# Kernel tuning notes

Hardware: AMD Instinct MI355X
Metric: run time of the kernel (lower is better)

## Reference

```python
import math
import jax, jax.numpy as jnp
import numpy as np

LMAX = 10
R_REF = 6371000.0
N = 1_000_000


def _sh_renorm(l, m, fourpi=True):
    base = math.sqrt((2.0 * l + 1.0) * math.factorial(l - abs(m)) / (4.0 * math.pi * math.factorial(l + abs(m))))
    if fourpi:
        base *= math.sqrt(4.0 * math.pi)
    return base


def _assoc_legendre(l, m, x):
    # P_l^m(x) via the standard stable recursion; l, m are Python ints (unrolled at trace time).
    pmm = jnp.ones_like(x)
    if m > 0:
        somx2 = jnp.sqrt(jnp.clip((1.0 - x) * (1.0 + x), 0.0, None))
        fact = 1.0
        for _ in range(1, m + 1):
            pmm = pmm * (-fact) * somx2
            fact += 2.0
    if l == m:
        return pmm
    pmmp1 = x * (2.0 * m + 1.0) * pmm
    if l == m + 1:
        return pmmp1
    pll = pmmp1
    for ll in range(m + 2, l + 1):
        pll = ((2.0 * ll - 1.0) * x * pmmp1 - (ll + m - 1.0) * pmm) / (ll - m)
        pmm = pmmp1
        pmmp1 = pll
    return pll


def _sh(m, l, phi, theta):
    cos_theta = jnp.clip(jnp.cos(theta), -1.0 + 1e-07, 1.0 - 1e-07)
    P_lm = _assoc_legendre(l, abs(m), cos_theta)
    K_lm = _sh_renorm(l, m)
    if m == 0:
        return K_lm * P_lm
    elif m > 0:
        return math.sqrt(2.0) * K_lm * jnp.cos(m * phi) * P_lm
    else:
        return math.sqrt(2.0) * K_lm * jnp.sin(-m * phi) * P_lm


def setup_inputs() -> dict:
    key = jax.random.key(0)
    k1, k2, k3 = jax.random.split(key, 3)
    lon = jax.random.uniform(k1, (N,), jnp.float32, -180.0, 180.0)
    lat = jax.random.uniform(k2, (N,), jnp.float32, -89.0, 89.0)
    r = R_REF * (1.0 + 0.01 * jax.random.uniform(k3, (N,), jnp.float32))
    return {"lonlatr": jnp.stack([lon, lat, r], axis=-1)}


def reference(lonlatr):
    lon, lat, r = lonlatr[:, 0], lonlatr[:, 1], lonlatr[:, 2]
    phi = jnp.deg2rad(lon + 180.0)
    theta = jnp.clip(jnp.deg2rad(90.0 - lat), 1e-07, math.pi - 1e-07)
    Y = []
    for l in range(LMAX + 1):
        for m in range(-l, l + 1):
            Y.append(_sh(m, l, phi, theta))
    Y = jnp.stack(Y, axis=-1)  # (N, (LMAX+1)^2)
    deg_idx = jnp.asarray(np.repeat(np.arange(LMAX + 1), 2 * np.arange(LMAX + 1) + 1), dtype=jnp.float32)
    radial_factor = (R_REF / r)[:, None] ** deg_idx[None, :]
    return Y * radial_factor
```

## Files before the change

### kernel.cpp

```cpp
#include <hip/hip_runtime.h>
#include <hip/hip_fp16.h>
#include <math.h>

#define LMAX 10
#define NCOL 121
#define PPB  64
#define TILEH (PPB * NCOL)
#define TILE4 (PPB * NCOL / 4)

typedef float f4_t __attribute__((ext_vector_type(4)));

struct Tab {
    float K[66];
    float A[66];
    float B[66];
};

template<int M, typename ST, typename EMIT>
__device__ __forceinline__ void chain(const Tab& t, ST* __restrict__ row,
                                      float pmm, float rfm, float rf, float x,
                                      float cm, float sm, EMIT emit) {
    {
        float v = t.K[M * (M + 1) / 2 + M] * pmm * rfm;
        if constexpr (M == 0) emit(row, 0, v);
        else { emit(row, M * M + 2 * M, v * cm); emit(row, M * M, v * sm); }
    }
    if constexpr (M < LMAX) {
        float p0 = pmm;
        float p1 = x * (float)(2 * M + 1) * pmm;
        float rfl = rfm * rf;
        {
            constexpr int L = M + 1;
            float v = t.K[L * (L + 1) / 2 + M] * p1 * rfl;
            if constexpr (M == 0) emit(row, L * L + L, v);
            else { emit(row, L * L + L + M, v * cm); emit(row, L * L + L - M, v * sm); }
        }
#pragma unroll
        for (int ll = M + 2; ll <= LMAX; ++ll) {
            int ti = ll * (ll + 1) / 2 + M;
            float p2 = t.A[ti] * x * p1 - t.B[ti] * p0;
            p0 = p1; p1 = p2;
            rfl *= rf;
            float v = t.K[ti] * p1 * rfl;
            int jb = ll * ll + ll;
            if constexpr (M == 0) emit(row, jb, v);
            else { emit(row, jb + M, v * cm); emit(row, jb - M, v * sm); }
        }
    }
}

template<typename ST, typename EMIT>
__device__ __forceinline__ void compute_tile(const float* __restrict__ in,
                                             long long gp, int s, const Tab& t,
                                             ST* __restrict__ row, EMIT emit) {
    const float lon = in[gp * 3 + 0];
    const float lat = in[gp * 3 + 1];
    const float r   = in[gp * 3 + 2];

    const float D2R  = 0.017453292519943295f;
    const float PI_F = 3.14159265358979323846f;

    float phi   = (lon + 180.0f) * D2R;
    float theta = fminf(fmaxf((90.0f - lat) * D2R, 1e-7f), PI_F - 1e-7f);
    float x = __cosf(theta);
    x = fminf(fmaxf(x, -1.0f + 1e-7f), 1.0f - 1e-7f);
    float somx2 = sqrtf(fmaxf((1.0f - x) * (1.0f + x), 0.0f));
    float rf  = 6371000.0f / r;
    float rf2 = rf * rf;
    float rf3 = rf2 * rf;
    float rf5 = rf3 * rf2;

    float c1, s1;
    __sincosf(phi, &s1, &c1);
    float c2 = c1 * c1 - s1 * s1, s2 = 2.0f * c1 * s1;
    float c3 = c2 * c1 - s2 * s1, s3 = s2 * c1 + c2 * s1;
    float c5 = (c2 * c2 - s2 * s2) * c1 - 2.0f * c2 * s2 * s1;
    float s5 = 2.0f * c2 * s2 * c1 + (c2 * c2 - s2 * s2) * s1;

    float sx2 = somx2 * somx2;
    float sx3 = sx2 * somx2;
    float sx5 = sx3 * sx2;

#define ROT(cm, sm, ck, sk) { float cn = cm * ck - sm * sk; sm = sm * ck + cm * sk; cm = cn; }
    switch (s) {
    case 0: {
        float pmm = 1.0f, rfm = 1.0f, cm = 1.0f, sm = 0.0f;
        chain<0>(t, row, pmm, rfm, rf, x, cm, sm, emit);
        pmm *= -945.0f    * sx5; rfm *= rf5; ROT(cm, sm, c5, s5);
        chain<5>(t, row, pmm, rfm, rf, x, cm, sm, emit);
        pmm *= -692835.0f * sx5; rfm *= rf5; ROT(cm, sm, c5, s5);
        chain<10>(t, row, pmm, rfm, rf, x, cm, sm, emit);
    } break;
    case 1: {
        float pmm = -somx2, rfm = rf, cm = c1, sm = s1;
        chain<1>(t, row, pmm, rfm, rf, x, cm, sm, emit);
        pmm *= -10395.0f * sx5; rfm *= rf5; ROT(cm, sm, c5, s5);
        chain<6>(t, row, pmm, rfm, rf, x, cm, sm, emit);
        pmm *= -3315.0f  * sx3; rfm *= rf3; ROT(cm, sm, c3, s3);
        chain<9>(t, row, pmm, rfm, rf, x, cm, sm, emit);
    } break;
    case 2: {
        float pmm = 3.0f * sx2, rfm = rf2, cm = c2, sm = s2;
        chain<2>(t, row, pmm, rfm, rf, x, cm, sm, emit);
        pmm *= -45045.0f * sx5; rfm *= rf5; ROT(cm, sm, c5, s5);
        chain<7>(t, row, pmm, rfm, rf, x, cm, sm, emit);
        pmm *= -15.0f * somx2;  rfm *= rf;  ROT(cm, sm, c1, s1);
        chain<8>(t, row, pmm, rfm, rf, x, cm, sm, emit);
    } break;
    default: {
        float pmm = -15.0f * sx3, rfm = rf3, cm = c3, sm = s3;
        chain<3>(t, row, pmm, rfm, rf, x, cm, sm, emit);
        pmm *= -7.0f * somx2; rfm *= rf; ROT(cm, sm, c1, s1);
        chain<4>(t, row, pmm, rfm, rf, x, cm, sm, emit);
    } break;
    }
#undef ROT
}

struct EmitH {
    __device__ void operator()(__half* row, int j, float v) const {
        row[j] = __float2half(v);
    }
};
struct EmitF {
    __device__ void operator()(float* row, int j, float v) const {
        row[j] = v;
    }
};

__device__ __forceinline__ void store_tile(const __half* __restrict__ buf,
                                           f4_t* __restrict__ dst) {
    const uint2* __restrict__ src = (const uint2*)buf;
#pragma unroll
    for (int k = 0; k < 7; ++k) {
        int i = threadIdx.x + k * 256;
        uint2 h = src[i];
        float2 fa = __half22float2(*(const __half2*)&h.x);
        float2 fb = __half22float2(*(const __half2*)&h.y);
        f4_t v = {fa.x, fa.y, fb.x, fb.y};
        __builtin_nontemporal_store(v, &dst[i]);
    }
    if (threadIdx.x < TILE4 - 7 * 256) {
        int i = threadIdx.x + 7 * 256;
        uint2 h = src[i];
        float2 fa = __half22float2(*(const __half2*)&h.x);
        float2 fb = __half22float2(*(const __half2*)&h.y);
        f4_t v = {fa.x, fa.y, fb.x, fb.y};
        __builtin_nontemporal_store(v, &dst[i]);
    }
}

__global__ __launch_bounds__(256, 5)
void sh_main(const float* __restrict__ in, float* __restrict__ out,
             int ntiles, Tab t) {
    __shared__ __half lds[2][TILEH];

    const int p = threadIdx.x & 63;
    const int s = threadIdx.x >> 6;

    int tile = blockIdx.x;
    if (tile >= ntiles) return;

    compute_tile(in, (long long)tile * PPB + p, s, t, &lds[0][p * NCOL], EmitH{});
    __syncthreads();

    int buf = 0;
    int prev = tile;
    for (tile += gridDim.x; tile < ntiles; tile += gridDim.x) {
        store_tile(lds[buf], (f4_t*)out + (long long)prev * TILE4);
        compute_tile(in, (long long)tile * PPB + p, s, t, &lds[buf ^ 1][p * NCOL], EmitH{});
        __syncthreads();
        buf ^= 1;
        prev = tile;
    }
    store_tile(lds[buf], (f4_t*)out + (long long)prev * TILE4);
}

__global__ __launch_bounds__(256)
void sh_tail(const float* __restrict__ in, float* __restrict__ out,
             int n, int tile0, Tab t) {
    __shared__ float lds[PPB * NCOL];
    const int p = threadIdx.x & 63;
    const int s = threadIdx.x >> 6;
    const long long gp = (long long)tile0 * PPB + p;
    if (gp < n)
        compute_tile(in, gp, s, t, &lds[p * NCOL], EmitF{});
    __syncthreads();
    const long long lim4 = ((long long)n * NCOL + 3) / 4;
    const long long base4 = (long long)tile0 * TILE4;
    f4_t* dst = (f4_t*)out + base4;
    const f4_t* src = (const f4_t*)lds;
    for (int f = threadIdx.x; f < TILE4; f += 256)
        if (base4 + f < lim4)
            __builtin_nontemporal_store(src[f], &dst[f]);
}

extern "C" void kernel_launch(void* const* d_in, const int* in_sizes, int n_in,
                              void* d_out, int out_size, void* d_ws, size_t ws_size,
                              hipStream_t stream) {
    const float* in = (const float*)d_in[0];
    float* out = (float*)d_out;
    const int n = in_sizes[0] / 3;

    Tab t;
    double fact[2 * LMAX + 1];
    fact[0] = 1.0;
    for (int i = 1; i <= 2 * LMAX; ++i) fact[i] = fact[i - 1] * (double)i;
    for (int l = 0; l <= LMAX; ++l) {
        for (int m = 0; m <= l; ++m) {
            int ti = l * (l + 1) / 2 + m;
            double k = sqrt((2.0 * l + 1.0) * fact[l - m] / fact[l + m]);
            if (m > 0) k *= sqrt(2.0);
            t.K[ti] = (float)k;
            if (l >= m + 2) {
                t.A[ti] = (float)((2.0 * l - 1.0) / (double)(l - m));
                t.B[ti] = (float)(((double)(l + m) - 1.0) / (double)(l - m));
            } else {
                t.A[ti] = 0.0f; t.B[ti] = 0.0f;
            }
        }
    }

    const int full_tiles = n / PPB;
    if (full_tiles > 0) {
        int nblk = full_tiles < 1280 ? full_tiles : 1280;
        sh_main<<<nblk, 256, 0, stream>>>(in, out, full_tiles, t);
    }
    if (n - full_tiles * PPB > 0)
        sh_tail<<<1, 256, 0, stream>>>(in, out, n, full_tiles, t);
}
```

Measured before the change: 103.0 us.

## Replace persistent double-buffered loop with one-tile-per-block grid launch

Drops the persistent-block scheme, where each block double-buffered tiles in LDS and overlapped storing one tile with computing the next. The kernel now launches one block per 64-point tile with a single LDS buffer and raises the occupancy hint from 5 to 8 blocks per CU. Overlap now comes from many resident blocks rather than in-block software pipelining, which halves LDS use per block. The cost is about 15.6k block launches, each paying its own setup and table-argument load.

```diff
diff --git a/kernel.cpp b/kernel.cpp
--- a/kernel.cpp
+++ b/kernel.cpp
@@ -128,9 +128,19 @@
     }
 };
 
-__device__ __forceinline__ void store_tile(const __half* __restrict__ buf,
-                                           f4_t* __restrict__ dst) {
-    const uint2* __restrict__ src = (const uint2*)buf;
+__global__ __launch_bounds__(256, 8)
+void sh_main(const float* __restrict__ in, float* __restrict__ out, Tab t) {
+    __shared__ __half lds[TILEH];
+
+    const int p = threadIdx.x & 63;
+    const int s = threadIdx.x >> 6;
+
+    compute_tile(in, (long long)blockIdx.x * PPB + p, s, t,
+                 &lds[p * NCOL], EmitH{});
+    __syncthreads();
+
+    f4_t* __restrict__ dst = (f4_t*)out + (long long)blockIdx.x * TILE4;
+    const uint2* __restrict__ src = (const uint2*)lds;
 #pragma unroll
     for (int k = 0; k < 7; ++k) {
         int i = threadIdx.x + k * 256;
@@ -148,32 +158,6 @@
         f4_t v = {fa.x, fa.y, fb.x, fb.y};
         __builtin_nontemporal_store(v, &dst[i]);
     }
-}
-
-__global__ __launch_bounds__(256, 5)
-void sh_main(const float* __restrict__ in, float* __restrict__ out,
-             int ntiles, Tab t) {
-    __shared__ __half lds[2][TILEH];
-
-    const int p = threadIdx.x & 63;
-    const int s = threadIdx.x >> 6;
-
-    int tile = blockIdx.x;
-    if (tile >= ntiles) return;
-
-    compute_tile(in, (long long)tile * PPB + p, s, t, &lds[0][p * NCOL], EmitH{});
-    __syncthreads();
-
-    int buf = 0;
-    int prev = tile;
-    for (tile += gridDim.x; tile < ntiles; tile += gridDim.x) {
-        store_tile(lds[buf], (f4_t*)out + (long long)prev * TILE4);
-        compute_tile(in, (long long)tile * PPB + p, s, t, &lds[buf ^ 1][p * NCOL], EmitH{});
-        __syncthreads();
-        buf ^= 1;
-        prev = tile;
-    }
-    store_tile(lds[buf], (f4_t*)out + (long long)prev * TILE4);
 }
 
 __global__ __launch_bounds__(256)
@@ -222,10 +206,8 @@
     }
 
     const int full_tiles = n / PPB;
-    if (full_tiles > 0) {
-        int nblk = full_tiles < 1280 ? full_tiles : 1280;
-        sh_main<<<nblk, 256, 0, stream>>>(in, out, full_tiles, t);
-    }
+    if (full_tiles > 0)
+        sh_main<<<full_tiles, 256, 0, stream>>>(in, out, t);
     if (n - full_tiles * PPB > 0)
         sh_tail<<<1, 256, 0, stream>>>(in, out, n, full_tiles, t);
 }
```

After: 97.65 us. -5.2%, faster.
